# Optimization experiments

Hardware: AMD Instinct MI355X
Metric: run time of the kernel (lower is better)

Reference implementation:

```python
import jax, jax.numpy as jnp
import numpy as np


def setup_inputs() -> dict:
    key = jax.random.key(0)
    k1, k2, k3, k4 = jax.random.split(key, 4)
    B, S, D = 8, 2048, 1024
    query = jax.random.normal(k1, (B, S, D), dtype=jnp.float32)
    key_t = jax.random.normal(k2, (B, S, D), dtype=jnp.float32)
    value = jax.random.normal(k3, (B, S, D), dtype=jnp.float32)
    # Dense(embed_dim) kernel/bias; NOTE: source (buggy but faithful) uses the
    # SAME query_linear weights for q, k, and v projections.
    Wq = jax.random.normal(k4, (D, D), dtype=jnp.float32) * (1.0 / np.sqrt(D))
    bq = jnp.zeros((D,), dtype=jnp.float32)
    return {"query": query, "key": key_t, "value": value, "Wq": Wq, "bq": bq}


def reference(query, key, value, Wq, bq):
    # All three projections use query_linear, matching the original source.
    q = query @ Wq + bq            # [B, S, D]
    k = key @ Wq + bq              # [B, S, D]
    v = value @ Wq + bq            # [B, S, D]
    dim_key = jnp.asarray(k.shape[-1], dtype=jnp.float32)
    logits = jnp.einsum('bqd,bkd->bqk', q, k) / jnp.sqrt(dim_key)  # [B, S, S]
    weights = jax.nn.softmax(logits, axis=-1)
    # dropout_rate = 0.0 / inference: dropout is identity
    out = jnp.einsum('bqk,bkd->bqd', weights, v)  # [B, S, D]
    return out
```

## Files before the change

kernel.cpp:

```cpp
#include <hip/hip_runtime.h>
#include <hip/hip_bf16.h>
#include <stdint.h>

typedef __attribute__((ext_vector_type(8))) short short8;
typedef __attribute__((ext_vector_type(4))) float f32x4;
typedef __attribute__((ext_vector_type(8))) unsigned short ushort8v;

__device__ __forceinline__ unsigned short f2bf(float f) {
  union { float f; uint32_t u; } v; v.f = f;
  uint32_t u = v.u;
  u += 0x7fffu + ((u >> 16) & 1u);
  return (unsigned short)(u >> 16);
}
__device__ __forceinline__ unsigned short f2h(float f) {
  union { _Float16 h; unsigned short u; } v; v.h = (_Float16)f; return v.u;
}
__device__ __forceinline__ float h2f(unsigned short u) {
  union { _Float16 h; unsigned short u; } v; v.u = u; return (float)v.h;
}

typedef const __attribute__((address_space(1))) unsigned int* gas_ptr;
typedef __attribute__((address_space(3))) unsigned int* las_ptr;

__device__ __forceinline__ void async16(const unsigned short* g, unsigned short* l) {
  __builtin_amdgcn_global_load_lds((gas_ptr)g, (las_ptr)l, 16, 0, 0);
}

#define FENCE() asm volatile("" ::: "memory")
#define BARRIER() do { FENCE(); __builtin_amdgcn_s_barrier(); FENCE(); } while (0)

#define BM 256
#define BN 256
#define BK 64
#define RGN 8192

template<int EPI>
__global__ __launch_bounds__(512, 2) void gemm256(
    const unsigned short* __restrict__ Abase,
    const unsigned short* __restrict__ Bbase,
    void* __restrict__ Cbase, const float* __restrict__ bias, float scale,
    int lda, int ldb, int ldc, int K, int mtiles, int ntiles,
    long long sA, long long sB, long long sC)
{
  __shared__ __align__(16) unsigned short lds[8 * RGN];

  const int tid  = threadIdx.x;
  const int nwg  = (int)gridDim.x;
  const int flat = (int)blockIdx.x;
  const int swz = (flat & 7) * (nwg >> 3) + (flat >> 3);
  const int per = mtiles * ntiles;
  const int z   = swz / per;
  const int rm  = swz - z * per;
  const int mb  = rm / ntiles;
  const int nb  = rm - mb * ntiles;
  const int m0  = mb * BM;
  const int n0  = nb * BN;

  const int wave = tid >> 6;
  const int lane = tid & 63;
  const int l16  = lane & 15;
  const int quad = lane >> 4;
  const int wm   = wave >> 2;
  const int wn   = wave & 3;

  const unsigned short* A = Abase + (size_t)z * (size_t)sA;
  const unsigned short* B = Bbase + (size_t)z * (size_t)sB;

  const int RA   = wm * 128 + l16;
  const int RB   = wn * 64  + l16;
  const int offA = RA * 32 + (quad ^ ((RA >> 1) & 3)) * 8;
  const int offB = RB * 32 + (quad ^ ((RB >> 1) & 3)) * 8;

  f32x4 acc[8][4] = {};

  const int nt = K / BK;

  auto stageA = [&](int kt, int h, int b) {
    unsigned short* rgn = lds + (size_t)(b * 4 + h) * RGN;
    #pragma unroll
    for (int i = 0; i < 2; ++i) {
      const int c  = i * 512 + tid;
      const int r  = c >> 2;
      const int s  = c & 3;
      const int sc = s ^ ((r >> 1) & 3);
      async16(A + (size_t)(m0 + r) * lda + kt * 64 + h * 32 + sc * 8,
              rgn + (size_t)(i * 512 + wave * 64) * 8);
    }
  };
  auto stageB = [&](int kt, int h, int b) {
    unsigned short* rgn = lds + (size_t)(b * 4 + 2 + h) * RGN;
    #pragma unroll
    for (int i = 0; i < 2; ++i) {
      const int c  = i * 512 + tid;
      const int r  = c >> 2;
      const int s  = c & 3;
      const int sc = s ^ ((r >> 1) & 3);
      async16(B + (size_t)(n0 + r) * ldb + kt * 64 + h * 32 + sc * 8,
              rgn + (size_t)(i * 512 + wave * 64) * 8);
    }
  };

  stageA(0, 0, 0); stageB(0, 0, 0); stageA(0, 1, 0); stageB(0, 1, 0);
  stageA(1, 0, 1); stageB(1, 0, 1); stageA(1, 1, 1);
  asm volatile("s_waitcnt vmcnt(6)" ::: "memory");
  BARRIER();

#define MFMA_QUAD(AF, BF, J0)                                                   \
  do {                                                                          \
    __builtin_amdgcn_s_setprio(1);                                              \
    _Pragma("unroll")                                                           \
    for (int mt = 0; mt < 8; ++mt) {                                            \
      acc[mt][J0]     = __builtin_amdgcn_mfma_f32_16x16x32_bf16(                \
          AF[mt], BF[J0],     acc[mt][J0],     0, 0, 0);                        \
      acc[mt][J0 + 1] = __builtin_amdgcn_mfma_f32_16x16x32_bf16(                \
          AF[mt], BF[J0 + 1], acc[mt][J0 + 1], 0, 0, 0);                        \
    }                                                                           \
    __builtin_amdgcn_s_setprio(0);                                              \
  } while (0)

  int cur = 0;
  for (int t = 0; t < nt; ++t, cur ^= 1) {
    const unsigned short* Ah0 = lds + (size_t)(cur * 4 + 0) * RGN;
    const unsigned short* Ah1 = Ah0 + RGN;
    const unsigned short* Bh0 = lds + (size_t)(cur * 4 + 2) * RGN;
    const unsigned short* Bh1 = Bh0 + RGN;

    short8 a0[8], a1[8], b0[4], b1[4];

    #pragma unroll
    for (int mt = 0; mt < 8; ++mt) a0[mt] = *(const short8*)&Ah0[offA + mt * 512];
    #pragma unroll
    for (int j = 0; j < 4; ++j)    b0[j]  = *(const short8*)&Bh0[offB + j * 512];
    if (t + 1 < nt) stageB(t + 1, 1, cur ^ 1);
    BARRIER();
    MFMA_QUAD(a0, b0, 0);
    BARRIER();

    #pragma unroll
    for (int mt = 0; mt < 8; ++mt) a1[mt] = *(const short8*)&Ah1[offA + mt * 512];
    if (t + 2 < nt) stageA(t + 2, 0, cur);
    BARRIER();
    MFMA_QUAD(a0, b0, 2);
    BARRIER();

    #pragma unroll
    for (int j = 0; j < 4; ++j) b1[j] = *(const short8*)&Bh1[offB + j * 512];
    if (t + 2 < nt) stageB(t + 2, 0, cur);
    BARRIER();
    MFMA_QUAD(a1, b1, 0);
    BARRIER();

    if (t + 2 < nt) stageA(t + 2, 1, cur);
    if (t < nt - 2)       asm volatile("s_waitcnt vmcnt(6)" ::: "memory");
    else if (t == nt - 2) asm volatile("s_waitcnt vmcnt(0)" ::: "memory");
    BARRIER();
    MFMA_QUAD(a1, b1, 2);
    BARRIER();
  }

  #pragma unroll
  for (int mt = 0; mt < 8; ++mt) {
    const int Rg = m0 + wm * 128 + mt * 16 + quad * 4;
    #pragma unroll
    for (int j = 0; j < 4; ++j) {
      const int Cg = n0 + wn * 64 + j * 16 + l16;
      float badd = 0.f;
      if (EPI == 0) badd = bias[Cg];
      #pragma unroll
      for (int r = 0; r < 4; ++r) {
        const size_t off = (size_t)z * (size_t)sC + (size_t)(Rg + r) * ldc + Cg;
        const float val = acc[mt][j][r];
        if (EPI == 0) {
          ((unsigned short*)Cbase)[off] = f2bf(val + badd);
        } else if (EPI == 1) {
          ((unsigned short*)Cbase)[off] = f2h(val * scale);
        } else {
          ((float*)Cbase)[off] = val * scale;
        }
      }
    }
  }
}

__global__ __launch_bounds__(256) void cvt3_bf16(
    const float* __restrict__ a, const float* __restrict__ b,
    const float* __restrict__ c,
    unsigned short* __restrict__ oa, unsigned short* __restrict__ ob,
    unsigned short* __restrict__ oc)
{
  const float* src = blockIdx.z == 0 ? a : (blockIdx.z == 1 ? b : c);
  unsigned short* dst = blockIdx.z == 0 ? oa : (blockIdx.z == 1 ? ob : oc);
  const size_t base = ((size_t)blockIdx.x * 256 + threadIdx.x) * 8;
  const float4 t0 = *(const float4*)(src + base);
  const float4 t1 = *(const float4*)(src + base + 4);
  ushort8v h;
  h[0] = f2bf(t0.x); h[1] = f2bf(t0.y); h[2] = f2bf(t0.z); h[3] = f2bf(t0.w);
  h[4] = f2bf(t1.x); h[5] = f2bf(t1.y); h[6] = f2bf(t1.z); h[7] = f2bf(t1.w);
  *(ushort8v*)(dst + base) = h;
}

__global__ __launch_bounds__(256) void transpose_w(
    const float* __restrict__ W, unsigned short* __restrict__ Wt)
{
  __shared__ float tile[64][65];
  const int k0 = blockIdx.x * 64;
  const int n0 = blockIdx.y * 64;
  #pragma unroll
  for (int i = 0; i < 16; ++i) {
    int lin = threadIdx.x + i * 256;
    int r = lin >> 6, c = lin & 63;
    tile[r][c] = W[(size_t)(k0 + r) * 1024 + n0 + c];
  }
  __syncthreads();
  #pragma unroll
  for (int i = 0; i < 16; ++i) {
    int lin = threadIdx.x + i * 256;
    int r = lin >> 6, c = lin & 63;
    Wt[(size_t)(n0 + r) * 1024 + k0 + c] = f2bf(tile[c][r]);
  }
}

__global__ __launch_bounds__(256) void transpose_v(
    const unsigned short* __restrict__ V, unsigned short* __restrict__ VT)
{
  __shared__ unsigned short tile[64][66];
  const int b  = blockIdx.z;
  const int s0 = blockIdx.x * 64;
  const int d0 = blockIdx.y * 64;
  const unsigned short* Vb  = V  + (size_t)b * 2048 * 1024;
  unsigned short*       VTb = VT + (size_t)b * 1024 * 2048;
  #pragma unroll
  for (int i = 0; i < 16; ++i) {
    int lin = threadIdx.x + i * 256;
    int r = lin >> 6, c = lin & 63;
    tile[r][c] = Vb[(size_t)(s0 + r) * 1024 + d0 + c];
  }
  __syncthreads();
  #pragma unroll
  for (int i = 0; i < 16; ++i) {
    int lin = threadIdx.x + i * 256;
    int r = lin >> 6, c = lin & 63;
    VTb[(size_t)(d0 + r) * 2048 + s0 + c] = tile[c][r];
  }
}

__global__ __launch_bounds__(256) void softmax_rows(
    const unsigned short* __restrict__ Lh, unsigned short* __restrict__ P)
{
  const int row  = blockIdx.x;
  const unsigned short* pin = Lh + (size_t)row * 2048;
  unsigned short*       pout = P + (size_t)row * 2048;
  const int tid  = threadIdx.x;
  const int lane = tid & 63;
  const int wave = tid >> 6;

  const ushort8v h = ((const ushort8v*)pin)[tid];
  float x[8];
  #pragma unroll
  for (int e = 0; e < 8; ++e) x[e] = h2f(h[e]);

  float mx = x[0];
  #pragma unroll
  for (int e = 1; e < 8; ++e) mx = fmaxf(mx, x[e]);
  #pragma unroll
  for (int o = 32; o > 0; o >>= 1) mx = fmaxf(mx, __shfl_xor(mx, o));
  __shared__ float redm[4];
  if (lane == 0) redm[wave] = mx;
  __syncthreads();
  mx = fmaxf(fmaxf(redm[0], redm[1]), fmaxf(redm[2], redm[3]));

  float s = 0.f;
  #pragma unroll
  for (int e = 0; e < 8; ++e) { x[e] = __expf(x[e] - mx); s += x[e]; }
  #pragma unroll
  for (int o = 32; o > 0; o >>= 1) s += __shfl_xor(s, o);
  __shared__ float reds[4];
  if (lane == 0) reds[wave] = s;
  __syncthreads();
  s = reds[0] + reds[1] + reds[2] + reds[3];

  const float inv = 1.0f / s;
  ushort8v o8;
  #pragma unroll
  for (int e = 0; e < 8; ++e) o8[e] = f2bf(x[e] * inv);
  ((ushort8v*)pout)[tid] = o8;
}

extern "C" void kernel_launch(void* const* d_in, const int* in_sizes, int n_in,
                              void* d_out, int out_size, void* d_ws, size_t ws_size,
                              hipStream_t stream)
{
  const float* query = (const float*)d_in[0];
  const float* key   = (const float*)d_in[1];
  const float* value = (const float*)d_in[2];
  const float* Wq    = (const float*)d_in[3];
  const float* bq    = (const float*)d_in[4];
  float* out = (float*)d_out;

  char* ws = (char*)d_ws;
  unsigned short* Wt  = (unsigned short*)(ws);
  unsigned short* Xq  = (unsigned short*)(ws + ((size_t)2   << 20));
  unsigned short* Xk  = (unsigned short*)(ws + ((size_t)34  << 20));
  unsigned short* Xv  = (unsigned short*)(ws + ((size_t)66  << 20));
  unsigned short* q   = (unsigned short*)(ws + ((size_t)98  << 20));
  unsigned short* v   = (unsigned short*)(ws + ((size_t)162 << 20));
  unsigned short* vT  = (unsigned short*)(ws + ((size_t)2   << 20));
  unsigned short* lgH = (unsigned short*)(ws + ((size_t)34  << 20));
  unsigned short* P   = (unsigned short*)(ws + ((size_t)98  << 20));

  transpose_w<<<dim3(16, 16, 1), 256, 0, stream>>>(Wq, Wt);
  cvt3_bf16<<<dim3(8192, 1, 3), 256, 0, stream>>>(query, key, value, Xq, Xk, Xv);

  gemm256<0><<<dim3(768, 1, 1), 512, 0, stream>>>(
      Xq, Wt, q, bq, 1.0f, 1024, 1024, 1024, 1024, 64, 4,
      (long long)16384 * 1024, 0, (long long)16384 * 1024);

  transpose_v<<<dim3(32, 16, 8), 256, 0, stream>>>(v, vT);

  gemm256<1><<<dim3(512, 1, 1), 512, 0, stream>>>(
      q, q + (size_t)32 * 1024 * 1024 / 2, lgH, nullptr, 0.03125f,
      1024, 1024, 2048, 1024, 8, 8,
      (long long)2048 * 1024, (long long)2048 * 1024, (long long)2048 * 2048);

  softmax_rows<<<dim3(8 * 2048, 1, 1), 256, 0, stream>>>(lgH, P);

  gemm256<2><<<dim3(256, 1, 1), 512, 0, stream>>>(
      P, vT, out, nullptr, 1.0f, 2048, 2048, 1024, 2048, 8, 4,
      (long long)2048 * 2048, (long long)1024 * 2048, (long long)2048 * 1024);
}
```

Before: 505.6 us.

## Restructure GEMM LDS layout into row-halves and interleave staging with MFMA quarters

```diff
diff --git a/kernel.cpp b/kernel.cpp
--- a/kernel.cpp
+++ b/kernel.cpp
@@ -66,96 +66,105 @@
   const unsigned short* A = Abase + (size_t)z * (size_t)sA;
   const unsigned short* B = Bbase + (size_t)z * (size_t)sB;
 
-  const int RA   = wm * 128 + l16;
-  const int RB   = wn * 64  + l16;
-  const int offA = RA * 32 + (quad ^ ((RA >> 1) & 3)) * 8;
-  const int offB = RB * 32 + (quad ^ ((RB >> 1) & 3)) * 8;
+  const int Kx  = (l16 >> 1) & 7;
+  const int sh0 = (quad ^ Kx) * 8;
+  const int sh1 = ((quad + 4) ^ Kx) * 8;
+  const int aOff = l16 * 64;
+  const int bOff = (wn & 1) * 4096 + l16 * 64;
 
   f32x4 acc[8][4] = {};
-
   const int nt = K / BK;
 
-  auto stageA = [&](int kt, int h, int b) {
-    unsigned short* rgn = lds + (size_t)(b * 4 + h) * RGN;
+  auto stage = [&](const unsigned short* S, int ldx, int rowBase, int kt, int rgn) {
+    unsigned short* dst = lds + (size_t)rgn * RGN;
     #pragma unroll
     for (int i = 0; i < 2; ++i) {
       const int c  = i * 512 + tid;
-      const int r  = c >> 2;
-      const int s  = c & 3;
-      const int sc = s ^ ((r >> 1) & 3);
-      async16(A + (size_t)(m0 + r) * lda + kt * 64 + h * 32 + sc * 8,
-              rgn + (size_t)(i * 512 + wave * 64) * 8);
+      const int r  = c >> 3;
+      const int s  = c & 7;
+      const int gc = s ^ ((r >> 1) & 7);
+      async16(S + (size_t)(rowBase + r) * ldx + kt * 64 + gc * 8,
+              dst + (size_t)c * 8);
     }
   };
-  auto stageB = [&](int kt, int h, int b) {
-    unsigned short* rgn = lds + (size_t)(b * 4 + 2 + h) * RGN;
-    #pragma unroll
-    for (int i = 0; i < 2; ++i) {
-      const int c  = i * 512 + tid;
-      const int r  = c >> 2;
-      const int s  = c & 3;
-      const int sc = s ^ ((r >> 1) & 3);
-      async16(B + (size_t)(n0 + r) * ldb + kt * 64 + h * 32 + sc * 8,
-              rgn + (size_t)(i * 512 + wave * 64) * 8);
+
+  short8 a[4][2], b0[2][2], b1[2][2];
+
+  auto readA = [&](const unsigned short* Ar, int qr) {
+    #pragma unroll
+    for (int mt = 0; mt < 4; ++mt) {
+      const int base = qr * 4096 + mt * 1024 + aOff;
+      a[mt][0] = *(const short8*)&Ar[base + sh0];
+      a[mt][1] = *(const short8*)&Ar[base + sh1];
     }
   };
-
-  stageA(0, 0, 0); stageB(0, 0, 0); stageA(0, 1, 0); stageB(0, 1, 0);
-  stageA(1, 0, 1); stageB(1, 0, 1); stageA(1, 1, 1);
+  auto readB = [&](const unsigned short* Br, int qc, short8 (&b)[2][2]) {
+    #pragma unroll
+    for (int ntl = 0; ntl < 2; ++ntl) {
+      const int base = bOff + qc * 2048 + ntl * 1024;
+      b[ntl][0] = *(const short8*)&Br[base + sh0];
+      b[ntl][1] = *(const short8*)&Br[base + sh1];
+    }
+  };
+  auto mfmaQ = [&](int qr, int qc, short8 (&b)[2][2]) {
+    __builtin_amdgcn_s_setprio(1);
+    #pragma unroll
+    for (int h = 0; h < 2; ++h)
+      #pragma unroll
+      for (int mt = 0; mt < 4; ++mt)
+        #pragma unroll
+        for (int ntl = 0; ntl < 2; ++ntl)
+          acc[qr * 4 + mt][qc * 2 + ntl] =
+              __builtin_amdgcn_mfma_f32_16x16x32_bf16(
+                  a[mt][h], b[ntl][h], acc[qr * 4 + mt][qc * 2 + ntl], 0, 0, 0);
+    __builtin_amdgcn_s_setprio(0);
+  };
+
+#define PHASE_SYNC() do { BARRIER();                                  \
+    asm volatile("s_waitcnt lgkmcnt(0)" ::: "memory");                \
+    __builtin_amdgcn_sched_barrier(0); } while (0)
+
+  stage(B, ldb, n0,       0, 2); stage(B, ldb, n0 + 128, 0, 3);
+  stage(A, lda, m0,       0, 0); stage(A, lda, m0 + 128, 0, 1);
+  stage(B, ldb, n0,       1, 6); stage(B, ldb, n0 + 128, 1, 7);
+  stage(A, lda, m0,       1, 4);
   asm volatile("s_waitcnt vmcnt(6)" ::: "memory");
   BARRIER();
 
-#define MFMA_QUAD(AF, BF, J0)                                                   \
-  do {                                                                          \
-    __builtin_amdgcn_s_setprio(1);                                              \
-    _Pragma("unroll")                                                           \
-    for (int mt = 0; mt < 8; ++mt) {                                            \
-      acc[mt][J0]     = __builtin_amdgcn_mfma_f32_16x16x32_bf16(                \
-          AF[mt], BF[J0],     acc[mt][J0],     0, 0, 0);                        \
-      acc[mt][J0 + 1] = __builtin_amdgcn_mfma_f32_16x16x32_bf16(                \
-          AF[mt], BF[J0 + 1], acc[mt][J0 + 1], 0, 0, 0);                        \
-    }                                                                           \
-    __builtin_amdgcn_s_setprio(0);                                              \
-  } while (0)
-
-  int cur = 0;
-  for (int t = 0; t < nt; ++t, cur ^= 1) {
-    const unsigned short* Ah0 = lds + (size_t)(cur * 4 + 0) * RGN;
-    const unsigned short* Ah1 = Ah0 + RGN;
-    const unsigned short* Bh0 = lds + (size_t)(cur * 4 + 2) * RGN;
-    const unsigned short* Bh1 = Bh0 + RGN;
-
-    short8 a0[8], a1[8], b0[4], b1[4];
-
-    #pragma unroll
-    for (int mt = 0; mt < 8; ++mt) a0[mt] = *(const short8*)&Ah0[offA + mt * 512];
-    #pragma unroll
-    for (int j = 0; j < 4; ++j)    b0[j]  = *(const short8*)&Bh0[offB + j * 512];
-    if (t + 1 < nt) stageB(t + 1, 1, cur ^ 1);
-    BARRIER();
-    MFMA_QUAD(a0, b0, 0);
-    BARRIER();
-
-    #pragma unroll
-    for (int mt = 0; mt < 8; ++mt) a1[mt] = *(const short8*)&Ah1[offA + mt * 512];
-    if (t + 2 < nt) stageA(t + 2, 0, cur);
-    BARRIER();
-    MFMA_QUAD(a0, b0, 2);
-    BARRIER();
-
-    #pragma unroll
-    for (int j = 0; j < 4; ++j) b1[j] = *(const short8*)&Bh1[offB + j * 512];
-    if (t + 2 < nt) stageB(t + 2, 0, cur);
-    BARRIER();
-    MFMA_QUAD(a1, b1, 0);
-    BARRIER();
-
-    if (t + 2 < nt) stageA(t + 2, 1, cur);
-    if (t < nt - 2)       asm volatile("s_waitcnt vmcnt(6)" ::: "memory");
-    else if (t == nt - 2) asm volatile("s_waitcnt vmcnt(0)" ::: "memory");
-    BARRIER();
-    MFMA_QUAD(a1, b1, 2);
-    BARRIER();
+  const unsigned short* A0r = lds + (size_t)(0 + wm) * RGN;
+  const unsigned short* B0r = lds + (size_t)(2 + (wn >> 1)) * RGN;
+  const unsigned short* A1r = lds + (size_t)(4 + wm) * RGN;
+  const unsigned short* B1r = lds + (size_t)(6 + (wn >> 1)) * RGN;
+
+  const int nit = nt >> 1;
+  for (int I = 0; I < nit; ++I) {
+    const int t0 = 2 * I, t1 = 2 * I + 1;
+    const bool st0 = (t0 + 2 < nt), st1 = (t1 + 2 < nt), last = (I == nit - 1);
+
+    readA(A0r, 0); readB(B0r, 0, b0);
+    stage(A, lda, m0 + 128, t1, 5);
+    PHASE_SYNC(); mfmaQ(0, 0, b0); BARRIER();
+    readB(B0r, 1, b1);
+    PHASE_SYNC(); mfmaQ(0, 1, b1); BARRIER();
+    readA(A0r, 1);
+    if (st0) { stage(B, ldb, n0, t0 + 2, 2); stage(B, ldb, n0 + 128, t0 + 2, 3); }
+    PHASE_SYNC(); mfmaQ(1, 0, b0); BARRIER();
+    if (st0) stage(A, lda, m0, t0 + 2, 0);
+    if (!last) asm volatile("s_waitcnt vmcnt(6)" ::: "memory");
+    else       asm volatile("s_waitcnt vmcnt(0)" ::: "memory");
+    PHASE_SYNC(); mfmaQ(1, 1, b1); BARRIER();
+
+    readA(A1r, 0); readB(B1r, 0, b0);
+    if (st0) stage(A, lda, m0 + 128, t0 + 2, 1);
+    PHASE_SYNC(); mfmaQ(0, 0, b0); BARRIER();
+    readB(B1r, 1, b1);
+    PHASE_SYNC(); mfmaQ(0, 1, b1); BARRIER();
+    readA(A1r, 1);
+    if (st1) { stage(B, ldb, n0, t1 + 2, 6); stage(B, ldb, n0 + 128, t1 + 2, 7); }
+    PHASE_SYNC(); mfmaQ(1, 0, b0); BARRIER();
+    if (st1) stage(A, lda, m0, t1 + 2, 4);
+    if (!last) asm volatile("s_waitcnt vmcnt(6)" ::: "memory");
+    PHASE_SYNC(); mfmaQ(1, 1, b1); BARRIER();
   }
 
   #pragma unroll
```

After: 490.2 us. -3.1%, faster.
